# Optimization experiments

Hardware: AMD Instinct MI355X
Metric: run time of the kernel (lower is better)

Reference implementation:

```python
import jax, jax.numpy as jnp
import numpy as np

N_NODES = 50000
N_EDGES = 800000
IN_F, E_F, OUT_F = 128, 32, 128

def setup_inputs() -> dict:
    key = jax.random.key(0)
    ks = jax.random.split(key, 8)
    return {
        "h": jax.random.normal(ks[0], (N_NODES, IN_F), dtype=jnp.float32),
        "eftr": jax.random.normal(ks[1], (N_EDGES, E_F), dtype=jnp.float32),
        "weight": jax.random.normal(ks[2], (IN_F + E_F, OUT_F), dtype=jnp.float32) * (1.0 / np.sqrt(IN_F + E_F)),
        "W_w": jax.random.normal(ks[3], (OUT_F, IN_F + OUT_F), dtype=jnp.float32) * (1.0 / np.sqrt(IN_F + OUT_F)),
        "W_b": jax.random.normal(ks[4], (OUT_F,), dtype=jnp.float32) * 0.01,
        "bias": jnp.zeros((OUT_F,), dtype=jnp.float32),
        "src_idx": jax.random.randint(ks[5], (N_EDGES,), 0, N_NODES, dtype=jnp.int64) if jax.config.jax_enable_x64 else jax.random.randint(ks[5], (N_EDGES,), 0, N_NODES, dtype=jnp.int32),
        "dst_idx": jax.random.randint(ks[6], (N_EDGES,), 0, N_NODES, dtype=jnp.int32),
        "num_dst": N_NODES,
    }

def reference(h, eftr, weight, W_w, W_b, bias, src_idx, dst_idx, num_dst):
    # Segment-mean of concat([h[src], eftr]) over dst neighborhoods.
    # Sum node part and edge part separately (avoids materializing the concat mailbox).
    sum_h = jax.ops.segment_sum(h[src_idx], dst_idx, num_segments=num_dst)   # [D, IN_F]
    sum_e = jax.ops.segment_sum(eftr, dst_idx, num_segments=num_dst)        # [D, E_F]
    cnt = jax.ops.segment_sum(jnp.ones((dst_idx.shape[0],), h.dtype), dst_idx, num_segments=num_dst)
    denom = jnp.maximum(cnt, 1.0)[:, None]  # zero-degree nodes -> h_neigh = 0
    feat_mean = jnp.concatenate([sum_h / denom, sum_e / denom], axis=-1)    # [D, IN_F+E_F]
    h_neigh = feat_mean @ weight                                            # [D, OUT_F]
    h_dst = h[:num_dst]
    h_prime = jnp.concatenate([h_dst, h_neigh], axis=1) @ W_w.T + W_b       # Linear W
    h_prime = h_prime + bias
    return h_prime
```

## Files before the change

### kernel.cpp

```cpp
#include <hip/hip_runtime.h>

#define NN   50000
#define NE   800000
#define INF  128
#define EF   32
#define OUTF 128
#define KDIM 288
#define NBLK ((NN + 1023) / 1024)

typedef __attribute__((ext_vector_type(8))) short          short8;
typedef __attribute__((ext_vector_type(8))) unsigned short ushort8;
typedef __attribute__((ext_vector_type(4))) unsigned short ushort4v;
typedef __attribute__((ext_vector_type(4))) float          float4v;

__device__ __forceinline__ unsigned short f2bf(float f) {
    union { float f; unsigned int u; } c; c.f = f;
    const unsigned int r = (c.u + 0x7FFFu + ((c.u >> 16) & 1u)) >> 16;
    return (unsigned short)r;
}

__global__ void prep_pack_kernel(const float* __restrict__ weight,
                                 const float* __restrict__ W_w,
                                 const float* __restrict__ W_b,
                                 const float* __restrict__ bias,
                                 unsigned short* __restrict__ Mb,
                                 float* __restrict__ cvec) {
    const int b = blockIdx.x;
    const int lane = threadIdx.x;
    if (b == 72) {
        cvec[lane]      = W_b[lane]      + bias[lane];
        cvec[lane + 64] = W_b[lane + 64] + bias[lane + 64];
        return;
    }
    const int kb = b >> 3;
    const int ct = b & 7;
    const int col = ct * 16 + (lane & 15);
    const int k0 = kb * 32 + (lane >> 4) * 8;
    ushort8 v;
#pragma unroll
    for (int i = 0; i < 8; ++i) {
        const int k = k0 + i;
        float val;
        if (k < 128) {
            val = W_w[(size_t)col * 256 + k];
        } else {
            const float4* wr  = (const float4*)(weight + (size_t)(k - 128) * OUTF);
            const float4* wwr = (const float4*)(W_w + (size_t)col * 256 + 128);
            float acc = 0.f;
#pragma unroll 4
            for (int c = 0; c < 32; ++c) {
                const float4 a = wr[c], bb = wwr[c];
                acc += a.x * bb.x + a.y * bb.y + a.z * bb.z + a.w * bb.w;
            }
            val = acc;
        }
        v[i] = f2bf(val);
    }
    *(ushort8*)(Mb + ((size_t)(b * 64 + lane) * 8)) = v;
}

__global__ __launch_bounds__(256)
void hist_kernel(const int* __restrict__ dst, int* __restrict__ off) {
    const int e = (blockIdx.x * 256 + threadIdx.x) * 4;
    if (e + 3 < NE) {
        const int4 d = *(const int4*)(dst + e);
        atomicAdd(&off[d.x], 1);
        atomicAdd(&off[d.y], 1);
        atomicAdd(&off[d.z], 1);
        atomicAdd(&off[d.w], 1);
    } else {
        for (int i = e; i < NE; ++i) atomicAdd(&off[dst[i]], 1);
    }
}

__global__ __launch_bounds__(256)
void scan1_kernel(const int* __restrict__ off, int* __restrict__ partial) {
    const int b = blockIdx.x;
    const int tid = threadIdx.x;
    const int idx = b * 1024 + tid * 4;
    int v0 = 0, v1 = 0, v2 = 0, v3 = 0;
    if (idx + 3 < NN) {
        const int4 q = *(const int4*)(off + idx);
        v0 = q.x; v1 = q.y; v2 = q.z; v3 = q.w;
    } else {
        if (idx + 0 < NN) v0 = off[idx + 0];
        if (idx + 1 < NN) v1 = off[idx + 1];
        if (idx + 2 < NN) v2 = off[idx + 2];
    }
    int t = v0 + v1 + v2 + v3;
#pragma unroll
    for (int ofs = 32; ofs > 0; ofs >>= 1) t += __shfl_down(t, ofs);
    __shared__ int wsum[4];
    if ((tid & 63) == 0) wsum[tid >> 6] = t;
    __syncthreads();
    if (tid == 0) partial[b] = wsum[0] + wsum[1] + wsum[2] + wsum[3];
}

__global__ __launch_bounds__(256)
void scan3_kernel(int* __restrict__ off, const int* __restrict__ partial) {
    __shared__ int blockbase;
    __shared__ int wsum[4];
    const int b = blockIdx.x;
    const int tid = threadIdx.x;
    const int lane = tid & 63;
    const int wid = tid >> 6;

    if (wid == 0) {
        const int v = (lane < NBLK) ? partial[lane] : 0;
        int x = v;
#pragma unroll
        for (int ofs = 1; ofs < 64; ofs <<= 1) {
            const int t = __shfl_up(x, ofs);
            if (lane >= ofs) x += t;
        }
        if (lane == b) blockbase = x - v;
    }

    const int idx = b * 1024 + tid * 4;
    int v0 = 0, v1 = 0, v2 = 0, v3 = 0;
    if (idx + 3 < NN) {
        const int4 q = *(const int4*)(off + idx);
        v0 = q.x; v1 = q.y; v2 = q.z; v3 = q.w;
    } else {
        if (idx + 0 < NN) v0 = off[idx + 0];
        if (idx + 1 < NN) v1 = off[idx + 1];
        if (idx + 2 < NN) v2 = off[idx + 2];
    }
    const int tsum = v0 + v1 + v2 + v3;
    int x = tsum;
#pragma unroll
    for (int ofs = 1; ofs < 64; ofs <<= 1) {
        const int t = __shfl_up(x, ofs);
        if (lane >= ofs) x += t;
    }
    if (lane == 63) wsum[wid] = x;
    __syncthreads();
    int wp = 0;
    for (int w = 0; w < wid; ++w) wp += wsum[w];
    const int base = blockbase + wp + (x - tsum);
    if (idx + 0 < NN) off[idx + 0] = base;
    if (idx + 1 < NN) off[idx + 1] = base + v0;
    if (idx + 2 < NN) off[idx + 2] = base + v0 + v1;
    if (idx + 3 < NN) off[idx + 3] = base + v0 + v1 + v2;
}

__global__ __launch_bounds__(256)
void scatter_ids_kernel(const int* __restrict__ srcv,
                        const int* __restrict__ dst,
                        int* __restrict__ off,
                        int2* __restrict__ eo2) {
    const int e = blockIdx.x * 256 + threadIdx.x;
    if (e < NE) {
        const int d = dst[e];
        const int pos = atomicAdd(&off[d], 1);
        eo2[pos] = make_int2(srcv[e], e);
    }
}

__global__ __launch_bounds__(256)
void gather_kernel(const float* __restrict__ h,
                   const float* __restrict__ eftr,
                   const int* __restrict__ off,
                   const int2* __restrict__ eo2,
                   unsigned short* __restrict__ mean_h,
                   unsigned short* __restrict__ mean_e) {
    const int tid = threadIdx.x;
    const int lane = tid & 63;
    const int node = blockIdx.x * 4 + (tid >> 6);
    if (node >= NN) return;

    const int end = off[node];
    const int start = (node == 0) ? 0 : off[node - 1];

    const int half = lane >> 5;
    const int hcol = (lane & 31) * 4;
    const int g = lane >> 3;
    const int ecol = (lane & 7) * 4;

    float4 ah = make_float4(0.f, 0.f, 0.f, 0.f);
    float4 ae = make_float4(0.f, 0.f, 0.f, 0.f);

    for (int base = start; base < end; base += 64) {
        const int m = min(64, end - base);
        int px = 0, py = 0;
        if (base + lane < end) {
            const long long pv =
                __builtin_nontemporal_load((const long long*)(eo2 + base + lane));
            px = (int)pv;
            py = (int)(pv >> 32);
        }
        for (int j = 0; j < m; j += 8) {
            float4 hv[4];
            bool hok[4];
#pragma unroll
            for (int u = 0; u < 4; ++u) {
                const int ei = j + 2 * u + half;
                const int s = __shfl(px, ei);
                hv[u] = *(const float4*)(h + (size_t)s * INF + hcol);
                hok[u] = (ei < m);
            }
            const int ee = __shfl(py, j + g);
            const float4 fv = *(const float4*)(eftr + (size_t)ee * EF + ecol);
            const bool eok = (j + g < m);
#pragma unroll
            for (int u = 0; u < 4; ++u)
                if (hok[u]) {
                    ah.x += hv[u].x; ah.y += hv[u].y;
                    ah.z += hv[u].z; ah.w += hv[u].w;
                }
            if (eok) {
                ae.x += fv.x; ae.y += fv.y; ae.z += fv.z; ae.w += fv.w;
            }
        }
    }

    ah.x += __shfl_xor(ah.x, 32); ah.y += __shfl_xor(ah.y, 32);
    ah.z += __shfl_xor(ah.z, 32); ah.w += __shfl_xor(ah.w, 32);
#pragma unroll
    for (int d = 8; d <= 32; d <<= 1) {
        ae.x += __shfl_xor(ae.x, d); ae.y += __shfl_xor(ae.y, d);
        ae.z += __shfl_xor(ae.z, d); ae.w += __shfl_xor(ae.w, d);
    }

    const float inv = 1.f / fmaxf((float)(end - start), 1.f);
    if (lane < 32) {
        ushort4v o;
        o[0] = f2bf(ah.x * inv); o[1] = f2bf(ah.y * inv);
        o[2] = f2bf(ah.z * inv); o[3] = f2bf(ah.w * inv);
        *(ushort4v*)(mean_h + (size_t)node * INF + hcol) = o;
    }
    if (lane < 8) {
        ushort4v o;
        o[0] = f2bf(ae.x * inv); o[1] = f2bf(ae.y * inv);
        o[2] = f2bf(ae.z * inv); o[3] = f2bf(ae.w * inv);
        *(ushort4v*)(mean_e + (size_t)node * EF + ecol) = o;
    }
}

__global__ __launch_bounds__(256)
void node_gemm_kernel(const float* __restrict__ h,
                      const unsigned short* __restrict__ mean_h,
                      const unsigned short* __restrict__ mean_e,
                      const unsigned short* __restrict__ Mb,
                      const float* __restrict__ cvec,
                      float* __restrict__ out) {
    const int tid = threadIdx.x;
    const int lane = tid & 63;
    const int wid = tid >> 6;
    const int nt = blockIdx.x * 4 + wid;
    const int m16 = lane & 15;
    const int quad = lane >> 4;
    const int koff = quad * 8;

    const int anode = nt * 16 + m16;
    const int nclamp = (anode < NN) ? anode : (NN - 1);

    float4v acc[8] = {};

    for (int kb = 0; kb < 9; ++kb) {
        short8 a;
        if (kb < 4) {
            const float* srcp = h + (size_t)nclamp * INF + kb * 32 + koff;
            const float4 p0 = *(const float4*)srcp;
            const float4 p1 = *(const float4*)(srcp + 4);
            a[0] = (short)f2bf(p0.x); a[1] = (short)f2bf(p0.y);
            a[2] = (short)f2bf(p0.z); a[3] = (short)f2bf(p0.w);
            a[4] = (short)f2bf(p1.x); a[5] = (short)f2bf(p1.y);
            a[6] = (short)f2bf(p1.z); a[7] = (short)f2bf(p1.w);
        } else if (kb < 8) {
            a = *(const short8*)(mean_h + (size_t)nclamp * INF + (kb - 4) * 32 + koff);
        } else {
            a = *(const short8*)(mean_e + (size_t)nclamp * EF + koff);
        }

        const short8* bp = (const short8*)(Mb + (size_t)kb * 8 * 64 * 8);
#pragma unroll
        for (int ct = 0; ct < 8; ++ct) {
            const short8 b = bp[ct * 64 + lane];
            acc[ct] = __builtin_amdgcn_mfma_f32_16x16x32_bf16(a, b, acc[ct], 0, 0, 0);
        }
    }

    float cv[8];
#pragma unroll
    for (int ct = 0; ct < 8; ++ct) cv[ct] = cvec[ct * 16 + m16];

#pragma unroll
    for (int r = 0; r < 4; ++r) {
        const int nrow = nt * 16 + quad * 4 + r;
        if (nrow < NN) {
            float* orow = out + (size_t)nrow * OUTF;
#pragma unroll
            for (int ct = 0; ct < 8; ++ct)
                orow[ct * 16 + m16] = acc[ct][r] + cv[ct];
        }
    }
}

extern "C" void kernel_launch(void* const* d_in, const int* in_sizes, int n_in,
                              void* d_out, int out_size, void* d_ws, size_t ws_size,
                              hipStream_t stream) {
    const float* h      = (const float*)d_in[0];
    const float* eftr   = (const float*)d_in[1];
    const float* weight = (const float*)d_in[2];
    const float* W_w    = (const float*)d_in[3];
    const float* W_b    = (const float*)d_in[4];
    const float* bias   = (const float*)d_in[5];
    const int*   src    = (const int*)d_in[6];
    const int*   dst    = (const int*)d_in[7];
    float* out = (float*)d_out;

    char* p = (char*)d_ws;
    unsigned short* mean_h = (unsigned short*)p;  p += (size_t)NN * INF * 2;
    unsigned short* mean_e = (unsigned short*)p;  p += (size_t)NN * EF * 2;
    unsigned short* Mb     = (unsigned short*)p;  p += (size_t)KDIM * OUTF * 2;
    float*          cvec   = (float*)p;          p += OUTF * 4;
    int*            off    = (int*)p;            p += (size_t)NN * 4;
    int2*           eo2    = (int2*)p;           p += (size_t)NE * 8;
    int*            partial= (int*)p;

    hipMemsetAsync(off, 0, (size_t)NN * sizeof(int), stream);

    prep_pack_kernel<<<73, 64, 0, stream>>>(weight, W_w, W_b, bias, Mb, cvec);
    hist_kernel<<<(NE / 4 + 255) / 256, 256, 0, stream>>>(dst, off);
    scan1_kernel<<<NBLK, 256, 0, stream>>>(off, partial);
    scan3_kernel<<<NBLK, 256, 0, stream>>>(off, partial);
    scatter_ids_kernel<<<(NE + 255) / 256, 256, 0, stream>>>(src, dst, off, eo2);
    gather_kernel<<<(NN + 3) / 4, 256, 0, stream>>>(h, eftr, off, eo2,
                                                    mean_h, mean_e);
    node_gemm_kernel<<<(NN / 64) + 1, 256, 0, stream>>>(h, mean_h, mean_e,
                                                        Mb, cvec, out);
}
```

Baseline: 352.2 us.

## Pre-convert node features to bf16 and gather bf16 rows in aggregation

```diff
diff --git a/kernel.cpp b/kernel.cpp
--- a/kernel.cpp
+++ b/kernel.cpp
@@ -18,15 +18,40 @@
     const unsigned int r = (c.u + 0x7FFFu + ((c.u >> 16) & 1u)) >> 16;
     return (unsigned short)r;
 }
+__device__ __forceinline__ float bf2f(unsigned short u) {
+    union { unsigned int u; float f; } c; c.u = ((unsigned int)u) << 16;
+    return c.f;
+}
+
+__global__ __launch_bounds__(256)
+void h2bf_kernel(const float* __restrict__ h, unsigned short* __restrict__ hb) {
+    const size_t i = ((size_t)blockIdx.x * 256 + threadIdx.x) * 8;
+    const float4 a = *(const float4*)(h + i);
+    const float4 b = *(const float4*)(h + i + 4);
+    ushort8 o;
+    o[0] = f2bf(a.x); o[1] = f2bf(a.y); o[2] = f2bf(a.z); o[3] = f2bf(a.w);
+    o[4] = f2bf(b.x); o[5] = f2bf(b.y); o[6] = f2bf(b.z); o[7] = f2bf(b.w);
+    *(ushort8*)(hb + i) = o;
+}
 
 __global__ void prep_pack_kernel(const float* __restrict__ weight,
                                  const float* __restrict__ W_w,
                                  const float* __restrict__ W_b,
                                  const float* __restrict__ bias,
                                  unsigned short* __restrict__ Mb,
-                                 float* __restrict__ cvec) {
+                                 float* __restrict__ cvec,
+                                 int* __restrict__ off) {
     const int b = blockIdx.x;
     const int lane = threadIdx.x;
+    if (b >= 73) {
+        const int idx = ((b - 73) * 64 + lane) * 4;
+        if (idx + 3 < NN) {
+            *(int4*)(off + idx) = make_int4(0, 0, 0, 0);
+        } else {
+            for (int i = idx; i < NN; ++i) off[i] = 0;
+        }
+        return;
+    }
     if (b == 72) {
         cvec[lane]      = W_b[lane]      + bias[lane];
         cvec[lane + 64] = W_b[lane + 64] + bias[lane + 64];
@@ -61,16 +86,8 @@
 
 __global__ __launch_bounds__(256)
 void hist_kernel(const int* __restrict__ dst, int* __restrict__ off) {
-    const int e = (blockIdx.x * 256 + threadIdx.x) * 4;
-    if (e + 3 < NE) {
-        const int4 d = *(const int4*)(dst + e);
-        atomicAdd(&off[d.x], 1);
-        atomicAdd(&off[d.y], 1);
-        atomicAdd(&off[d.z], 1);
-        atomicAdd(&off[d.w], 1);
-    } else {
-        for (int i = e; i < NE; ++i) atomicAdd(&off[dst[i]], 1);
-    }
+    const int e = blockIdx.x * 256 + threadIdx.x;
+    if (e < NE) atomicAdd(&off[dst[e]], 1);
 }
 
 __global__ __launch_bounds__(256)
@@ -158,7 +175,7 @@
 }
 
 __global__ __launch_bounds__(256)
-void gather_kernel(const float* __restrict__ h,
+void gather_kernel(const unsigned short* __restrict__ hb,
                    const float* __restrict__ eftr,
                    const int* __restrict__ off,
                    const int2* __restrict__ eo2,
@@ -172,12 +189,12 @@
     const int end = off[node];
     const int start = (node == 0) ? 0 : off[node - 1];
 
-    const int half = lane >> 5;
-    const int hcol = (lane & 31) * 4;
-    const int g = lane >> 3;
+    const int gh = lane >> 4;
+    const int hcol = (lane & 15) * 8;
+    const int ge = lane >> 3;
     const int ecol = (lane & 7) * 4;
 
-    float4 ah = make_float4(0.f, 0.f, 0.f, 0.f);
+    float ah[8] = {};
     float4 ae = make_float4(0.f, 0.f, 0.f, 0.f);
 
     for (int base = start; base < end; base += 64) {
@@ -190,32 +207,34 @@
             py = (int)(pv >> 32);
         }
         for (int j = 0; j < m; j += 8) {
-            float4 hv[4];
-            bool hok[4];
-#pragma unroll
-            for (int u = 0; u < 4; ++u) {
-                const int ei = j + 2 * u + half;
-                const int s = __shfl(px, ei);
-                hv[u] = *(const float4*)(h + (size_t)s * INF + hcol);
-                hok[u] = (ei < m);
+            const int i0 = j + gh;
+            const int i1 = j + 4 + gh;
+            const int s0 = __shfl(px, i0);
+            const int s1 = __shfl(px, i1);
+            const ushort8 r0 = *(const ushort8*)(hb + (size_t)s0 * INF + hcol);
+            const ushort8 r1 = *(const ushort8*)(hb + (size_t)s1 * INF + hcol);
+            const float w0 = (i0 < m) ? 1.f : 0.f;
+            const float w1 = (i1 < m) ? 1.f : 0.f;
+            const int ee = __shfl(py, j + ge);
+            const float4 fv = *(const float4*)(eftr + (size_t)ee * EF + ecol);
+            const float we = (j + ge < m) ? 1.f : 0.f;
+#pragma unroll
+            for (int i = 0; i < 8; ++i) {
+                ah[i] = fmaf(w0, bf2f(r0[i]), ah[i]);
+                ah[i] = fmaf(w1, bf2f(r1[i]), ah[i]);
             }
-            const int ee = __shfl(py, j + g);
-            const float4 fv = *(const float4*)(eftr + (size_t)ee * EF + ecol);
-            const bool eok = (j + g < m);
-#pragma unroll
-            for (int u = 0; u < 4; ++u)
-                if (hok[u]) {
-                    ah.x += hv[u].x; ah.y += hv[u].y;
-                    ah.z += hv[u].z; ah.w += hv[u].w;
-                }
-            if (eok) {
-                ae.x += fv.x; ae.y += fv.y; ae.z += fv.z; ae.w += fv.w;
-            }
-        }
-    }
-
-    ah.x += __shfl_xor(ah.x, 32); ah.y += __shfl_xor(ah.y, 32);
-    ah.z += __shfl_xor(ah.z, 32); ah.w += __shfl_xor(ah.w, 32);
+            ae.x = fmaf(we, fv.x, ae.x);
+            ae.y = fmaf(we, fv.y, ae.y);
+            ae.z = fmaf(we, fv.z, ae.z);
+            ae.w = fmaf(we, fv.w, ae.w);
+        }
+    }
+
+#pragma unroll
+    for (int i = 0; i < 8; ++i) {
+        ah[i] += __shfl_xor(ah[i], 16);
+        ah[i] += __shfl_xor(ah[i], 32);
+    }
 #pragma unroll
     for (int d = 8; d <= 32; d <<= 1) {
         ae.x += __shfl_xor(ae.x, d); ae.y += __shfl_xor(ae.y, d);
@@ -223,11 +242,11 @@
     }
 
     const float inv = 1.f / fmaxf((float)(end - start), 1.f);
-    if (lane < 32) {
-        ushort4v o;
-        o[0] = f2bf(ah.x * inv); o[1] = f2bf(ah.y * inv);
-        o[2] = f2bf(ah.z * inv); o[3] = f2bf(ah.w * inv);
-        *(ushort4v*)(mean_h + (size_t)node * INF + hcol) = o;
+    if (lane < 16) {
+        ushort8 o;
+#pragma unroll
+        for (int i = 0; i < 8; ++i) o[i] = f2bf(ah[i] * inv);
+        *(ushort8*)(mean_h + (size_t)node * INF + lane * 8) = o;
     }
     if (lane < 8) {
         ushort4v o;
@@ -238,7 +257,7 @@
 }
 
 __global__ __launch_bounds__(256)
-void node_gemm_kernel(const float* __restrict__ h,
+void node_gemm_kernel(const unsigned short* __restrict__ hb,
                       const unsigned short* __restrict__ mean_h,
                       const unsigned short* __restrict__ mean_e,
                       const unsigned short* __restrict__ Mb,
@@ -259,19 +278,12 @@
 
     for (int kb = 0; kb < 9; ++kb) {
         short8 a;
-        if (kb < 4) {
-            const float* srcp = h + (size_t)nclamp * INF + kb * 32 + koff;
-            const float4 p0 = *(const float4*)srcp;
-            const float4 p1 = *(const float4*)(srcp + 4);
-            a[0] = (short)f2bf(p0.x); a[1] = (short)f2bf(p0.y);
-            a[2] = (short)f2bf(p0.z); a[3] = (short)f2bf(p0.w);
-            a[4] = (short)f2bf(p1.x); a[5] = (short)f2bf(p1.y);
-            a[6] = (short)f2bf(p1.z); a[7] = (short)f2bf(p1.w);
-        } else if (kb < 8) {
+        if (kb < 4)
+            a = *(const short8*)(hb + (size_t)nclamp * INF + kb * 32 + koff);
+        else if (kb < 8)
             a = *(const short8*)(mean_h + (size_t)nclamp * INF + (kb - 4) * 32 + koff);
-        } else {
+        else
             a = *(const short8*)(mean_e + (size_t)nclamp * EF + koff);
-        }
 
         const short8* bp = (const short8*)(Mb + (size_t)kb * 8 * 64 * 8);
 #pragma unroll
@@ -311,23 +323,23 @@
     float* out = (float*)d_out;
 
     char* p = (char*)d_ws;
+    unsigned short* hb     = (unsigned short*)p;  p += (size_t)NN * INF * 2;
     unsigned short* mean_h = (unsigned short*)p;  p += (size_t)NN * INF * 2;
     unsigned short* mean_e = (unsigned short*)p;  p += (size_t)NN * EF * 2;
     unsigned short* Mb     = (unsigned short*)p;  p += (size_t)KDIM * OUTF * 2;
-    float*          cvec   = (float*)p;          p += OUTF * 4;
-    int*            off    = (int*)p;            p += (size_t)NN * 4;
-    int2*           eo2    = (int2*)p;           p += (size_t)NE * 8;
+    float*          cvec   = (float*)p;           p += OUTF * 4;
+    int*            off    = (int*)p;             p += (size_t)NN * 4;
+    int2*           eo2    = (int2*)p;            p += (size_t)NE * 8;
     int*            partial= (int*)p;
 
-    hipMemsetAsync(off, 0, (size_t)NN * sizeof(int), stream);
-
-    prep_pack_kernel<<<73, 64, 0, stream>>>(weight, W_w, W_b, bias, Mb, cvec);
-    hist_kernel<<<(NE / 4 + 255) / 256, 256, 0, stream>>>(dst, off);
+    h2bf_kernel<<<3125, 256, 0, stream>>>(h, hb);
+    prep_pack_kernel<<<269, 64, 0, stream>>>(weight, W_w, W_b, bias, Mb, cvec, off);
+    hist_kernel<<<(NE + 255) / 256, 256, 0, stream>>>(dst, off);
     scan1_kernel<<<NBLK, 256, 0, stream>>>(off, partial);
     scan3_kernel<<<NBLK, 256, 0, stream>>>(off, partial);
     scatter_ids_kernel<<<(NE + 255) / 256, 256, 0, stream>>>(src, dst, off, eo2);
-    gather_kernel<<<(NN + 3) / 4, 256, 0, stream>>>(h, eftr, off, eo2,
+    gather_kernel<<<(NN + 3) / 4, 256, 0, stream>>>(hb, eftr, off, eo2,
                                                     mean_h, mean_e);
-    node_gemm_kernel<<<(NN / 64) + 1, 256, 0, stream>>>(h, mean_h, mean_e,
+    node_gemm_kernel<<<(NN / 64) + 1, 256, 0, stream>>>(hb, mean_h, mean_e,
                                                         Mb, cvec, out);
 }
```

New measurement: 343.3 us. 1.03x faster.
